# Optimization experiments

Measured on AMD Instinct MI355X. Metric: run time of the kernel, lower is better.

The kernel has to match this reference:

```python
import jax, jax.numpy as jnp
import numpy as np

N_NODES = 50000
N_EDGES = 800000
D_IN = 512
LATENT = [512, 512, 512]
L2_EPS = 1e-12  # torch F.normalize clamp_min


def _gin_layer(x, src, dst, W, b, eps):
    # sum aggregation of neighbor (source) features into destination nodes
    agg = jax.ops.segment_sum(x[src], dst, num_segments=x.shape[0])  # [N, d]
    h = agg + (1.0 + eps) * x
    return jax.nn.relu(h @ W + b)  # Sequential(Linear, ReLU)


def _l2_normalize(x):
    n = jnp.sqrt(jnp.sum(x * x, axis=-1, keepdims=True))
    return x / jnp.maximum(n, L2_EPS)


def setup_inputs() -> dict:
    key = jax.random.key(0)
    ks = jax.random.split(key, 10)
    x = jax.random.normal(ks[0], (N_NODES, D_IN), dtype=jnp.float32)
    edge_index = jax.random.randint(ks[1], (2, N_EDGES), 0, N_NODES, dtype=jnp.int32)
    dims = [D_IN] + LATENT
    inp = {"x": x, "edge_index": edge_index}
    for i in range(3):
        fan_in = dims[i]
        bound = 1.0 / np.sqrt(fan_in)
        inp[f"W{i+1}"] = jax.random.uniform(ks[2 + 2 * i], (dims[i], dims[i + 1]), jnp.float32, -bound, bound)
        inp[f"b{i+1}"] = jax.random.uniform(ks[3 + 2 * i], (dims[i + 1],), jnp.float32, -bound, bound)
        inp[f"eps{i+1}"] = jnp.zeros((), dtype=jnp.float32)  # train_eps=True, init 0
    return inp


def reference(x, edge_index, W1, b1, eps1, W2, b2, eps2, W3, b3, eps3):
    src, dst = edge_index[0], edge_index[1]
    # layers 0..num_layers-2: GINConv -> L2 normalize -> ReLU
    h = _gin_layer(x, src, dst, W1, b1, eps1)
    h = jax.nn.relu(_l2_normalize(h))
    h = _gin_layer(h, src, dst, W2, b2, eps2)
    h = jax.nn.relu(_l2_normalize(h))
    # final layer: raw GINConv output = logits
    logits = _gin_layer(h, src, dst, W3, b3, eps3)
    probs = jax.nn.softmax(logits, axis=-1)
    return (logits, probs)
```

## Files before the change

### kernel.cpp

```cpp
#include <hip/hip_runtime.h>
#include <stdint.h>

#define N_NODES 50000
#define N_EDGES 800000

typedef unsigned int uint32;

__device__ inline float bflo(uint32 u) { return __builtin_bit_cast(float, u << 16); }
__device__ inline float bfhi(uint32 u) { return __builtin_bit_cast(float, u & 0xffff0000u); }
__device__ inline float bf2f(unsigned short h) { return __builtin_bit_cast(float, (uint32)h << 16); }
__device__ inline unsigned short f2bf(float f) {
    uint32 u = __builtin_bit_cast(uint32, f);
    u += 0x7fffu + ((u >> 16) & 1u);
    return (unsigned short)(u >> 16);
}
__device__ inline uint32 pack2(float lo, float hi) {
    return (uint32)f2bf(lo) | ((uint32)f2bf(hi) << 16);
}

__global__ __launch_bounds__(256) void zero_k(int* p, int n) {
    int i = blockIdx.x * 256 + threadIdx.x;
    if (i < n) p[i] = 0;
}

__global__ __launch_bounds__(256) void count_k(const int* __restrict__ ei, int* __restrict__ cnt) {
    int e = blockIdx.x * 256 + threadIdx.x;
    if (e < N_EDGES) atomicAdd(&cnt[ei[N_EDGES + e]], 1);
}

#define NB 196

__global__ __launch_bounds__(256) void blocksum_k(const int* __restrict__ cnt, int* __restrict__ bsum) {
    int i = blockIdx.x * 256 + threadIdx.x;
    int v = (i < N_NODES) ? cnt[i] : 0;
#pragma unroll
    for (int off = 32; off > 0; off >>= 1) v += __shfl_down(v, off);
    __shared__ int sh[4];
    int w = threadIdx.x >> 6, lane = threadIdx.x & 63;
    if (lane == 0) sh[w] = v;
    __syncthreads();
    if (threadIdx.x == 0) bsum[blockIdx.x] = sh[0] + sh[1] + sh[2] + sh[3];
}

__global__ __launch_bounds__(256) void bscan_k(const int* __restrict__ bsum, int* __restrict__ bpre,
                                               int* __restrict__ rowptr) {
    __shared__ int sh[256];
    int t = threadIdx.x;
    int v = (t < NB) ? bsum[t] : 0;
    sh[t] = v;
    __syncthreads();
    for (int d = 1; d < 256; d <<= 1) {
        int u = (t >= d) ? sh[t - d] : 0;
        __syncthreads();
        sh[t] += u;
        __syncthreads();
    }
    if (t < NB) bpre[t] = sh[t] - v;
    if (t == NB - 1) rowptr[N_NODES] = sh[t];
}

__global__ __launch_bounds__(256) void scatter_k(int* __restrict__ cnt, const int* __restrict__ bpre,
                                                 int* __restrict__ rowptr) {
    int b = blockIdx.x, t = threadIdx.x, i = b * 256 + t;
    int w = t >> 6, lane = t & 63;
    int myv = (i < N_NODES) ? cnt[i] : 0;
    int v = myv;
#pragma unroll
    for (int d = 1; d < 64; d <<= 1) {
        int u = __shfl_up(v, d);
        if (lane >= d) v += u;
    }
    __shared__ int wt[4];
    if (lane == 63) wt[w] = v;
    __syncthreads();
    int off = bpre[b];
    for (int k = 0; k < w; k++) off += wt[k];
    int excl = v - myv + off;
    if (i < N_NODES) {
        rowptr[i] = excl;
        cnt[i] = excl;
    }
}

__global__ __launch_bounds__(256) void fill_k(const int* __restrict__ ei, int* __restrict__ cursor,
                                              int* __restrict__ csr) {
    int e = blockIdx.x * 256 + threadIdx.x;
    if (e < N_EDGES) {
        int d = ei[N_EDGES + e];
        int p = atomicAdd(&cursor[d], 1);
        csr[p] = ei[e];
    }
}

__global__ __launch_bounds__(256) void wprep_k(const float* __restrict__ W,
                                               unsigned short* __restrict__ Whi,
                                               unsigned short* __restrict__ Wlo) {
    int idx = blockIdx.x * 256 + threadIdx.x;
    int k = idx >> 9, n = idx & 511;
    float w = W[idx];
    unsigned short hi = f2bf(w);
    float lo = w - bf2f(hi);
    Whi[n * 512 + k] = hi;
    Wlo[n * 512 + k] = f2bf(lo);
}

__global__ __launch_bounds__(256) void xconv_k(const float* __restrict__ x, uint32* __restrict__ xb) {
    int i = blockIdx.x * 256 + threadIdx.x;
    float2 v = ((const float2*)x)[i];
    xb[i] = pack2(v.x, v.y);
}

__global__ __launch_bounds__(256) void norm_k(const uint4* __restrict__ z, float* __restrict__ invn) {
    int node = blockIdx.x * 4 + (threadIdx.x >> 6);
    int lane = threadIdx.x & 63;
    uint4 q = z[(size_t)node * 64 + lane];
    float f0 = bflo(q.x), f1 = bfhi(q.x), f2 = bflo(q.y), f3 = bfhi(q.y);
    float f4 = bflo(q.z), f5 = bfhi(q.z), f6 = bflo(q.w), f7 = bfhi(q.w);
    float ss = f0 * f0 + f1 * f1 + f2 * f2 + f3 * f3 + f4 * f4 + f5 * f5 + f6 * f6 + f7 * f7;
#pragma unroll
    for (int off = 32; off > 0; off >>= 1) ss += __shfl_xor(ss, off);
    if (lane == 0) invn[node] = 1.0f / fmaxf(sqrtf(ss), 1e-12f);
}

template <bool SCALED>
__global__ __launch_bounds__(256) void agg_k(const uint4* __restrict__ xin,
                                             const int* __restrict__ rowptr,
                                             const int* __restrict__ csr,
                                             const float* __restrict__ eps,
                                             const float* __restrict__ invn,
                                             uint4* __restrict__ hout) {
    int node = blockIdx.x * 4 + (threadIdx.x >> 6);
    int lane = threadIdx.x & 63;
    int beg = rowptr[node], end = rowptr[node + 1];
    float a0 = 0.f, a1 = 0.f, a2 = 0.f, a3 = 0.f, a4 = 0.f, a5 = 0.f, a6 = 0.f, a7 = 0.f;
    int e = beg;
    for (; e + 4 <= end; e += 4) {
        int s0 = csr[e], s1 = csr[e + 1], s2 = csr[e + 2], s3 = csr[e + 3];
        uint4 q0 = xin[(size_t)s0 * 64 + lane];
        uint4 q1 = xin[(size_t)s1 * 64 + lane];
        uint4 q2 = xin[(size_t)s2 * 64 + lane];
        uint4 q3 = xin[(size_t)s3 * 64 + lane];
        float w0 = SCALED ? invn[s0] : 1.0f;
        float w1 = SCALED ? invn[s1] : 1.0f;
        float w2 = SCALED ? invn[s2] : 1.0f;
        float w3 = SCALED ? invn[s3] : 1.0f;
        a0 = fmaf(w0, bflo(q0.x), fmaf(w1, bflo(q1.x), fmaf(w2, bflo(q2.x), fmaf(w3, bflo(q3.x), a0))));
        a1 = fmaf(w0, bfhi(q0.x), fmaf(w1, bfhi(q1.x), fmaf(w2, bfhi(q2.x), fmaf(w3, bfhi(q3.x), a1))));
        a2 = fmaf(w0, bflo(q0.y), fmaf(w1, bflo(q1.y), fmaf(w2, bflo(q2.y), fmaf(w3, bflo(q3.y), a2))));
        a3 = fmaf(w0, bfhi(q0.y), fmaf(w1, bfhi(q1.y), fmaf(w2, bfhi(q2.y), fmaf(w3, bfhi(q3.y), a3))));
        a4 = fmaf(w0, bflo(q0.z), fmaf(w1, bflo(q1.z), fmaf(w2, bflo(q2.z), fmaf(w3, bflo(q3.z), a4))));
        a5 = fmaf(w0, bfhi(q0.z), fmaf(w1, bfhi(q1.z), fmaf(w2, bfhi(q2.z), fmaf(w3, bfhi(q3.z), a5))));
        a6 = fmaf(w0, bflo(q0.w), fmaf(w1, bflo(q1.w), fmaf(w2, bflo(q2.w), fmaf(w3, bflo(q3.w), a6))));
        a7 = fmaf(w0, bfhi(q0.w), fmaf(w1, bfhi(q1.w), fmaf(w2, bfhi(q2.w), fmaf(w3, bfhi(q3.w), a7))));
    }
    for (; e < end; ++e) {
        int s0 = csr[e];
        uint4 q0 = xin[(size_t)s0 * 64 + lane];
        float w0 = SCALED ? invn[s0] : 1.0f;
        a0 = fmaf(w0, bflo(q0.x), a0); a1 = fmaf(w0, bfhi(q0.x), a1);
        a2 = fmaf(w0, bflo(q0.y), a2); a3 = fmaf(w0, bfhi(q0.y), a3);
        a4 = fmaf(w0, bflo(q0.z), a4); a5 = fmaf(w0, bfhi(q0.z), a5);
        a6 = fmaf(w0, bflo(q0.w), a6); a7 = fmaf(w0, bfhi(q0.w), a7);
    }
    uint4 qs = xin[(size_t)node * 64 + lane];
    float ws = (1.0f + eps[0]) * (SCALED ? invn[node] : 1.0f);
    a0 = fmaf(ws, bflo(qs.x), a0); a1 = fmaf(ws, bfhi(qs.x), a1);
    a2 = fmaf(ws, bflo(qs.y), a2); a3 = fmaf(ws, bfhi(qs.y), a3);
    a4 = fmaf(ws, bflo(qs.z), a4); a5 = fmaf(ws, bfhi(qs.z), a5);
    a6 = fmaf(ws, bflo(qs.w), a6); a7 = fmaf(ws, bfhi(qs.w), a7);
    uint4 o;
    o.x = pack2(a0, a1);
    o.y = pack2(a2, a3);
    o.z = pack2(a4, a5);
    o.w = pack2(a6, a7);
    hout[(size_t)node * 64 + lane] = o;
}

typedef __bf16 bf16x8 __attribute__((ext_vector_type(8)));
typedef float f32x4 __attribute__((ext_vector_type(4)));

__device__ inline void async16(const void* g, void* l) {
    __builtin_amdgcn_global_load_lds((const __attribute__((address_space(1))) void*)g,
                                     (__attribute__((address_space(3))) void*)l, 16, 0, 0);
}

template <bool SPLIT, bool F32OUT>
__global__ __launch_bounds__(256) void gemm_k(const unsigned short* __restrict__ A,
                                              const unsigned short* __restrict__ Whi,
                                              const unsigned short* __restrict__ Wlo,
                                              const float* __restrict__ bias,
                                              unsigned short* __restrict__ outB,
                                              float* __restrict__ outF, int M) {
    constexpr int K = 512, N = 512, BK = 32, TM = 128;
    __shared__ unsigned short lds_a[TM * BK];
    __shared__ unsigned short lds_bh[TM * BK];
    __shared__ unsigned short lds_bl[SPLIT ? TM * BK : 16];
    const int t = threadIdx.x;
    const int w = t >> 6, lane = t & 63;
    const int wrow = w >> 1, wcol = w & 1;
    const int m0 = blockIdx.y * TM;
    const int n0 = blockIdx.x * TM;

    int r0 = w * 16 + (lane >> 2), cc = (lane & 3) * 8;
    int r1 = 64 + r0;
    int am0 = m0 + r0; am0 = am0 < M ? am0 : M - 1;
    int am1 = m0 + r1; am1 = am1 < M ? am1 : M - 1;
    const unsigned short* ag0 = A + (size_t)am0 * K + cc;
    const unsigned short* ag1 = A + (size_t)am1 * K + cc;
    const unsigned short* bh0 = Whi + (size_t)(n0 + r0) * K + cc;
    const unsigned short* bh1 = Whi + (size_t)(n0 + r1) * K + cc;
    const unsigned short* bl0 = Wlo + (size_t)(n0 + r0) * K + cc;
    const unsigned short* bl1 = Wlo + (size_t)(n0 + r1) * K + cc;
    unsigned short* la0 = lds_a + w * 512;
    unsigned short* la1 = lds_a + 2048 + w * 512;
    unsigned short* lh0 = lds_bh + w * 512;
    unsigned short* lh1 = lds_bh + 2048 + w * 512;
    unsigned short* ll0 = lds_bl + w * 512;
    unsigned short* ll1 = lds_bl + 2048 + w * 512;

    f32x4 acc[4][4] = {};
    const int quad = lane >> 4, l15 = lane & 15;
    const int arow = wrow * 64 + l15;
    const int brow = wcol * 64 + l15;

    for (int k0 = 0; k0 < K; k0 += BK) {
        __syncthreads();
        async16(ag0 + k0, la0);
        async16(ag1 + k0, la1);
        async16(bh0 + k0, lh0);
        async16(bh1 + k0, lh1);
        if (SPLIT) {
            async16(bl0 + k0, ll0);
            async16(bl1 + k0, ll1);
        }
        __syncthreads();
        bf16x8 af[4], bh[4], bl[4];
#pragma unroll
        for (int i = 0; i < 4; i++)
            af[i] = *(const bf16x8*)&lds_a[(arow + i * 16) * BK + quad * 8];
#pragma unroll
        for (int j = 0; j < 4; j++)
            bh[j] = *(const bf16x8*)&lds_bh[(brow + j * 16) * BK + quad * 8];
        if (SPLIT) {
#pragma unroll
            for (int j = 0; j < 4; j++)
                bl[j] = *(const bf16x8*)&lds_bl[(brow + j * 16) * BK + quad * 8];
        }
#pragma unroll
        for (int i = 0; i < 4; i++)
#pragma unroll
            for (int j = 0; j < 4; j++) {
                acc[i][j] = __builtin_amdgcn_mfma_f32_16x16x32_bf16(af[i], bh[j], acc[i][j], 0, 0, 0);
                if (SPLIT)
                    acc[i][j] = __builtin_amdgcn_mfma_f32_16x16x32_bf16(af[i], bl[j], acc[i][j], 0, 0, 0);
            }
    }

#pragma unroll
    for (int j = 0; j < 4; j++) {
        int n = n0 + wcol * 64 + j * 16 + l15;
        float bv = bias[n];
#pragma unroll
        for (int i = 0; i < 4; i++) {
            int mbase = m0 + wrow * 64 + i * 16 + quad * 4;
#pragma unroll
            for (int r = 0; r < 4; r++) {
                int m = mbase + r;
                if (m < M) {
                    float v = fmaxf(acc[i][j][r] + bv, 0.0f);
                    if (F32OUT) outF[(size_t)m * N + n] = v;
                    else        outB[(size_t)m * N + n] = f2bf(v);
                }
            }
        }
    }
}

__global__ __launch_bounds__(256) void softmax_k(const float* __restrict__ logits,
                                                 float* __restrict__ probs) {
    int node = blockIdx.x * 4 + (threadIdx.x >> 6);
    int lane = threadIdx.x & 63;
    const float4* zp = (const float4*)(logits + (size_t)node * 512);
    float4 q0 = zp[lane * 2], q1 = zp[lane * 2 + 1];
    float f[8] = {q0.x, q0.y, q0.z, q0.w, q1.x, q1.y, q1.z, q1.w};
    float m = f[0];
#pragma unroll
    for (int i = 1; i < 8; i++) m = fmaxf(m, f[i]);
#pragma unroll
    for (int off = 32; off > 0; off >>= 1) m = fmaxf(m, __shfl_xor(m, off));
    float e[8], s = 0.f;
#pragma unroll
    for (int i = 0; i < 8; i++) { e[i] = __expf(f[i] - m); s += e[i]; }
#pragma unroll
    for (int off = 32; off > 0; off >>= 1) s += __shfl_xor(s, off);
    float inv = 1.0f / s;
    float4* pp = (float4*)(probs + (size_t)node * 512);
    pp[lane * 2]     = make_float4(e[0] * inv, e[1] * inv, e[2] * inv, e[3] * inv);
    pp[lane * 2 + 1] = make_float4(e[4] * inv, e[5] * inv, e[6] * inv, e[7] * inv);
}

extern "C" void kernel_launch(void* const* d_in, const int* in_sizes, int n_in,
                              void* d_out, int out_size, void* d_ws, size_t ws_size,
                              hipStream_t stream) {
    (void)in_sizes; (void)n_in; (void)out_size; (void)ws_size;
    const float* x = (const float*)d_in[0];
    const int* ei = (const int*)d_in[1];
    const float* W1 = (const float*)d_in[2];
    const float* b1 = (const float*)d_in[3];
    const float* e1 = (const float*)d_in[4];
    const float* W2 = (const float*)d_in[5];
    const float* b2 = (const float*)d_in[6];
    const float* e2 = (const float*)d_in[7];
    const float* W3 = (const float*)d_in[8];
    const float* b3 = (const float*)d_in[9];
    const float* e3 = (const float*)d_in[10];
    float* out = (float*)d_out;
    float* out_logits = out;
    float* out_probs = out + (size_t)N_NODES * 512;

    char* ws = (char*)d_ws;
    int* rowptr = (int*)ws;
    int* cursor = rowptr + 50048;
    int* csr = cursor + 50048;
    float* invn = (float*)(csr + N_EDGES);
    int* bsum = (int*)(invn + 50048);
    int* bpre = bsum + 256;
    unsigned short* Wsp = (unsigned short*)(bpre + 256);
    unsigned short* featA = Wsp + 3 * 524288;
    unsigned short* featB = featA + (size_t)N_NODES * 512;

    zero_k<<<196, 256, 0, stream>>>(cursor, N_NODES);
    count_k<<<(N_EDGES + 255) / 256, 256, 0, stream>>>(ei, cursor);
    blocksum_k<<<NB, 256, 0, stream>>>(cursor, bsum);
    bscan_k<<<1, 256, 0, stream>>>(bsum, bpre, rowptr);
    scatter_k<<<NB, 256, 0, stream>>>(cursor, bpre, rowptr);
    fill_k<<<(N_EDGES + 255) / 256, 256, 0, stream>>>(ei, cursor, csr);

    wprep_k<<<1024, 256, 0, stream>>>(W1, Wsp,           Wsp + 262144);
    wprep_k<<<1024, 256, 0, stream>>>(W2, Wsp + 524288,  Wsp + 786432);
    wprep_k<<<1024, 256, 0, stream>>>(W3, Wsp + 1048576, Wsp + 1310720);

    xconv_k<<<50000, 256, 0, stream>>>(x, (uint32*)featB);

    dim3 ggrid(4, (N_NODES + 127) / 128);

    agg_k<false><<<12500, 256, 0, stream>>>((const uint4*)featB, rowptr, csr, e1, nullptr, (uint4*)featA);
    gemm_k<false, false><<<ggrid, 256, 0, stream>>>(featA, Wsp, Wsp + 262144, b1, featB, nullptr, N_NODES);
    norm_k<<<12500, 256, 0, stream>>>((const uint4*)featB, invn);
    agg_k<true><<<12500, 256, 0, stream>>>((const uint4*)featB, rowptr, csr, e2, invn, (uint4*)featA);
    gemm_k<false, false><<<ggrid, 256, 0, stream>>>(featA, Wsp + 524288, Wsp + 786432, b2, featB, nullptr, N_NODES);
    norm_k<<<12500, 256, 0, stream>>>((const uint4*)featB, invn);
    agg_k<true><<<12500, 256, 0, stream>>>((const uint4*)featB, rowptr, csr, e3, invn, (uint4*)featA);
    gemm_k<true, true><<<ggrid, 256, 0, stream>>>(featA, Wsp + 1048576, Wsp + 1310720, b3, nullptr, out_logits, N_NODES);
    softmax_k<<<N_NODES / 4, 256, 0, stream>>>(out_logits, out_probs);
}
```

Baseline: 1.034 ms.

## Fuse L2 row sum-of-squares into GEMM epilogue, tile weight transpose, widen x conversion

```diff
diff --git a/kernel.cpp b/kernel.cpp
--- a/kernel.cpp
+++ b/kernel.cpp
@@ -95,31 +95,45 @@
 __global__ __launch_bounds__(256) void wprep_k(const float* __restrict__ W,
                                                unsigned short* __restrict__ Whi,
                                                unsigned short* __restrict__ Wlo) {
-    int idx = blockIdx.x * 256 + threadIdx.x;
-    int k = idx >> 9, n = idx & 511;
-    float w = W[idx];
-    unsigned short hi = f2bf(w);
-    float lo = w - bf2f(hi);
-    Whi[n * 512 + k] = hi;
-    Wlo[n * 512 + k] = f2bf(lo);
-}
-
-__global__ __launch_bounds__(256) void xconv_k(const float* __restrict__ x, uint32* __restrict__ xb) {
+    __shared__ float sh[64][65];
+    int bk = (blockIdx.x & 7) * 64;
+    int bn = (blockIdx.x >> 3) * 64;
+    int t = threadIdx.x;
+    int lr = t >> 4;
+    int lc4 = (t & 15) * 4;
+#pragma unroll
+    for (int i = 0; i < 4; i++) {
+        int k = lr + i * 16;
+        float4 v = *(const float4*)&W[(size_t)(bk + k) * 512 + bn + lc4];
+        sh[k][lc4] = v.x; sh[k][lc4 + 1] = v.y; sh[k][lc4 + 2] = v.z; sh[k][lc4 + 3] = v.w;
+    }
+    __syncthreads();
+#pragma unroll
+    for (int i = 0; i < 4; i++) {
+        int n = lr + i * 16;
+        float w0 = sh[lc4][n], w1 = sh[lc4 + 1][n], w2 = sh[lc4 + 2][n], w3 = sh[lc4 + 3][n];
+        ushort4 h, l;
+        h.x = f2bf(w0); l.x = f2bf(w0 - bf2f(h.x));
+        h.y = f2bf(w1); l.y = f2bf(w1 - bf2f(h.y));
+        h.z = f2bf(w2); l.z = f2bf(w2 - bf2f(h.z));
+        h.w = f2bf(w3); l.w = f2bf(w3 - bf2f(h.w));
+        *(ushort4*)&Whi[(size_t)(bn + n) * 512 + bk + lc4] = h;
+        *(ushort4*)&Wlo[(size_t)(bn + n) * 512 + bk + lc4] = l;
+    }
+}
+
+__global__ __launch_bounds__(256) void xconv_k(const float4* __restrict__ x, uint2* __restrict__ xb) {
     int i = blockIdx.x * 256 + threadIdx.x;
-    float2 v = ((const float2*)x)[i];
-    xb[i] = pack2(v.x, v.y);
-}
-
-__global__ __launch_bounds__(256) void norm_k(const uint4* __restrict__ z, float* __restrict__ invn) {
-    int node = blockIdx.x * 4 + (threadIdx.x >> 6);
-    int lane = threadIdx.x & 63;
-    uint4 q = z[(size_t)node * 64 + lane];
-    float f0 = bflo(q.x), f1 = bfhi(q.x), f2 = bflo(q.y), f3 = bfhi(q.y);
-    float f4 = bflo(q.z), f5 = bfhi(q.z), f6 = bflo(q.w), f7 = bfhi(q.w);
-    float ss = f0 * f0 + f1 * f1 + f2 * f2 + f3 * f3 + f4 * f4 + f5 * f5 + f6 * f6 + f7 * f7;
-#pragma unroll
-    for (int off = 32; off > 0; off >>= 1) ss += __shfl_xor(ss, off);
-    if (lane == 0) invn[node] = 1.0f / fmaxf(sqrtf(ss), 1e-12f);
+    float4 v = x[i];
+    uint2 o;
+    o.x = pack2(v.x, v.y);
+    o.y = pack2(v.z, v.w);
+    xb[i] = o;
+}
+
+__global__ __launch_bounds__(256) void invn_k(const float* __restrict__ ss, float* __restrict__ invn) {
+    int i = blockIdx.x * 256 + threadIdx.x;
+    if (i < N_NODES) invn[i] = 1.0f / fmaxf(sqrtf(ss[i]), 1e-12f);
 }
 
 template <bool SCALED>
@@ -184,13 +198,14 @@
                                      (__attribute__((address_space(3))) void*)l, 16, 0, 0);
 }
 
-template <bool SPLIT, bool F32OUT>
+template <bool SPLIT, bool F32OUT, bool NORM>
 __global__ __launch_bounds__(256) void gemm_k(const unsigned short* __restrict__ A,
                                               const unsigned short* __restrict__ Whi,
                                               const unsigned short* __restrict__ Wlo,
                                               const float* __restrict__ bias,
                                               unsigned short* __restrict__ outB,
-                                              float* __restrict__ outF, int M) {
+                                              float* __restrict__ outF,
+                                              float* __restrict__ ssOut, int M) {
     constexpr int K = 512, N = 512, BK = 32, TM = 128;
     __shared__ unsigned short lds_a[TM * BK];
     __shared__ unsigned short lds_bh[TM * BK];
@@ -257,20 +272,34 @@
     }
 
 #pragma unroll
-    for (int j = 0; j < 4; j++) {
-        int n = n0 + wcol * 64 + j * 16 + l15;
-        float bv = bias[n];
-#pragma unroll
-        for (int i = 0; i < 4; i++) {
-            int mbase = m0 + wrow * 64 + i * 16 + quad * 4;
+    for (int i = 0; i < 4; i++) {
+        int mbase = m0 + wrow * 64 + i * 16 + quad * 4;
+        float rs[4] = {0.f, 0.f, 0.f, 0.f};
+#pragma unroll
+        for (int j = 0; j < 4; j++) {
+            int n = n0 + wcol * 64 + j * 16 + l15;
+            float bv = bias[n];
 #pragma unroll
             for (int r = 0; r < 4; r++) {
                 int m = mbase + r;
                 if (m < M) {
                     float v = fmaxf(acc[i][j][r] + bv, 0.0f);
+                    if (NORM) rs[r] += v * v;
                     if (F32OUT) outF[(size_t)m * N + n] = v;
                     else        outB[(size_t)m * N + n] = f2bf(v);
                 }
+            }
+        }
+        if (NORM) {
+#pragma unroll
+            for (int r = 0; r < 4; r++) {
+                float s = rs[r];
+                s += __shfl_xor(s, 1);
+                s += __shfl_xor(s, 2);
+                s += __shfl_xor(s, 4);
+                s += __shfl_xor(s, 8);
+                int m = mbase + r;
+                if (l15 == 0 && m < M) atomicAdd(&ssOut[m], s);
             }
         }
     }
@@ -325,32 +354,36 @@
     float* invn = (float*)(csr + N_EDGES);
     int* bsum = (int*)(invn + 50048);
     int* bpre = bsum + 256;
-    unsigned short* Wsp = (unsigned short*)(bpre + 256);
+    float* ss = (float*)(bpre + 256);
+    float* ss1 = ss;
+    float* ss2 = ss + 50048;
+    unsigned short* Wsp = (unsigned short*)(ss + 2 * 50048);
     unsigned short* featA = Wsp + 3 * 524288;
     unsigned short* featB = featA + (size_t)N_NODES * 512;
 
     zero_k<<<196, 256, 0, stream>>>(cursor, N_NODES);
+    zero_k<<<392, 256, 0, stream>>>((int*)ss, 2 * 50048);
     count_k<<<(N_EDGES + 255) / 256, 256, 0, stream>>>(ei, cursor);
     blocksum_k<<<NB, 256, 0, stream>>>(cursor, bsum);
     bscan_k<<<1, 256, 0, stream>>>(bsum, bpre, rowptr);
     scatter_k<<<NB, 256, 0, stream>>>(cursor, bpre, rowptr);
     fill_k<<<(N_EDGES + 255) / 256, 256, 0, stream>>>(ei, cursor, csr);
 
-    wprep_k<<<1024, 256, 0, stream>>>(W1, Wsp,           Wsp + 262144);
-    wprep_k<<<1024, 256, 0, stream>>>(W2, Wsp + 524288,  Wsp + 786432);
-    wprep_k<<<1024, 256, 0, stream>>>(W3, Wsp + 1048576, Wsp + 1310720);
-
-    xconv_k<<<50000, 256, 0, stream>>>(x, (uint32*)featB);
+    wprep_k<<<64, 256, 0, stream>>>(W1, Wsp,           Wsp + 262144);
+    wprep_k<<<64, 256, 0, stream>>>(W2, Wsp + 524288,  Wsp + 786432);
+    wprep_k<<<64, 256, 0, stream>>>(W3, Wsp + 1048576, Wsp + 1310720);
+
+    xconv_k<<<25000, 256, 0, stream>>>((const float4*)x, (uint2*)featB);
 
     dim3 ggrid(4, (N_NODES + 127) / 128);
 
     agg_k<false><<<12500, 256, 0, stream>>>((const uint4*)featB, rowptr, csr, e1, nullptr, (uint4*)featA);
-    gemm_k<false, false><<<ggrid, 256, 0, stream>>>(featA, Wsp, Wsp + 262144, b1, featB, nullptr, N_NODES);
-    norm_k<<<12500, 256, 0, stream>>>((const uint4*)featB, invn);
+    gemm_k<false, false, true><<<ggrid, 256, 0, stream>>>(featA, Wsp, Wsp + 262144, b1, featB, nullptr, ss1, N_NODES);
+    invn_k<<<196, 256, 0, stream>>>(ss1, invn);
     agg_k<true><<<12500, 256, 0, stream>>>((const uint4*)featB, rowptr, csr, e2, invn, (uint4*)featA);
-    gemm_k<false, false><<<ggrid, 256, 0, stream>>>(featA, Wsp + 524288, Wsp + 786432, b2, featB, nullptr, N_NODES);
-    norm_k<<<12500, 256, 0, stream>>>((const uint4*)featB, invn);
+    gemm_k<false, false, true><<<ggrid, 256, 0, stream>>>(featA, Wsp + 524288, Wsp + 786432, b2, featB, nullptr, ss2, N_NODES);
+    invn_k<<<196, 256, 0, stream>>>(ss2, invn);
     agg_k<true><<<12500, 256, 0, stream>>>((const uint4*)featB, rowptr, csr, e3, invn, (uint4*)featA);
-    gemm_k<true, true><<<ggrid, 256, 0, stream>>>(featA, Wsp + 1048576, Wsp + 1310720, b3, nullptr, out_logits, N_NODES);
+    gemm_k<true, true, false><<<ggrid, 256, 0, stream>>>(featA, Wsp + 1048576, Wsp + 1310720, b3, nullptr, out_logits, nullptr, N_NODES);
     softmax_k<<<N_NODES / 4, 256, 0, stream>>>(out_logits, out_probs);
 }
```

After: 998.4 us. 1.04x faster.
